# Kernel tuning notes

Hardware: AMD Instinct MI355X
Metric: run time of the kernel (lower is better)

The kernel has to match this reference:

```python
import jax, jax.numpy as jnp
import numpy as np

EPS = 1e-12  # F.normalize eps

def _l2norm(x, axis=-1):
    n = jnp.linalg.norm(x, axis=axis, keepdims=True)
    return x / jnp.maximum(n, EPS)

def setup_inputs() -> dict:
    key = jax.random.key(0)
    k1, k2 = jax.random.split(key)
    Q, D = 512, 1024
    B, L = 64, 1024
    queries = jax.random.normal(k1, (Q, D), dtype=jnp.float32)
    local_tokens = jax.random.normal(k2, (B, L, D), dtype=jnp.float32)
    return {"queries": queries, "local_tokens": local_tokens}

def reference(queries, local_tokens):
    # sim_op == 'dot', repeat == True, need_attn_weights == False
    D = local_tokens.shape[-1]
    denom = jnp.sqrt(jnp.asarray(D, dtype=queries.dtype))
    # scores: [B, Q, L] == bmm(expand(queries), local_tokens^T) / sqrt(D)
    scores = jnp.einsum('qd,bld->bql', queries, local_tokens) / denom
    attn = jax.nn.softmax(scores, axis=-1)
    # aggregated: [B, Q, D]
    agg = jnp.einsum('bql,bld->bqd', attn, local_tokens)
    # post L2-normalize both sides (query normalize is batch-invariant)
    qn = _l2norm(queries)          # [Q, D]
    aggn = _l2norm(agg)            # [B, Q, D]
    # per-(b,q) dot product -> [B, Q], then transpose -> [Q, B]
    logits = jnp.einsum('qd,bqd->bq', qn, aggn).T
    return logits
```

## Files before the change

### kernel.cpp

```cpp
#include <hip/hip_runtime.h>
#include <stdint.h>

#define QN 512
#define DN 1024
#define BN 64
#define LN 1024

typedef _Float16 f16x8 __attribute__((ext_vector_type(8)));
typedef _Float16 f16x4 __attribute__((ext_vector_type(4)));
typedef float f32x4 __attribute__((ext_vector_type(4)));

#define DMA16(gp, lp)                                                        \
  __builtin_amdgcn_global_load_lds(                                          \
      (const __attribute__((address_space(1))) uint32_t*)(const void*)(gp),  \
      (__attribute__((address_space(3))) uint32_t*)(void*)(lp), 16, 0, 0)

#define WAITVM0() asm volatile("s_waitcnt vmcnt(0)" ::: "memory")

__global__ __launch_bounds__(256) void k_convert(const float* __restrict__ tok,
                                                 _Float16* __restrict__ T,
                                                 _Float16* __restrict__ TT) {
  __shared__ __align__(16) _Float16 tile[64][68];
  const int b = blockIdx.z;
  const int l0 = blockIdx.y * 64, d0 = blockIdx.x * 64;
  const int tid = threadIdx.x;
  const int rr = tid >> 4;
  const int cq = tid & 15;
  const size_t base = (size_t)b * LN * DN;
#pragma unroll
  for (int p = 0; p < 4; ++p) {
    const int l = p * 16 + rr;
    const float4 v = *(const float4*)(tok + base + (size_t)(l0 + l) * DN + d0 + cq * 4);
    f16x4 hv;
    hv[0] = (_Float16)v.x; hv[1] = (_Float16)v.y; hv[2] = (_Float16)v.z; hv[3] = (_Float16)v.w;
    *(f16x4*)(T + base + (size_t)(l0 + l) * DN + d0 + cq * 4) = hv;
    tile[cq * 4 + 0][l] = hv[0];
    tile[cq * 4 + 1][l] = hv[1];
    tile[cq * 4 + 2][l] = hv[2];
    tile[cq * 4 + 3][l] = hv[3];
  }
  __syncthreads();
  const size_t baseT = (size_t)b * DN * LN;
#pragma unroll
  for (int p = 0; p < 4; ++p) {
    const int d = p * 16 + rr;
    const f16x4 hv = *(const f16x4*)(&tile[d][cq * 4]);
    *(f16x4*)(TT + baseT + (size_t)(d0 + d) * LN + l0 + cq * 4) = hv;
  }
}

__global__ __launch_bounds__(256) void k_queries(const float* __restrict__ q,
                                                 _Float16* __restrict__ Qh,
                                                 float* __restrict__ invqn) {
  const int qr = blockIdx.x;
  const int tid = threadIdx.x;
  const float4 v = *(const float4*)(q + (size_t)qr * DN + tid * 4);
  float ss = v.x * v.x + v.y * v.y + v.z * v.z + v.w * v.w;
#pragma unroll
  for (int off = 1; off < 64; off <<= 1) ss += __shfl_xor(ss, off, 64);
  __shared__ float red[4];
  if ((tid & 63) == 0) red[tid >> 6] = ss;
  __syncthreads();
  const float tot = red[0] + red[1] + red[2] + red[3];
  f16x4 hv;
  hv[0] = (_Float16)v.x; hv[1] = (_Float16)v.y; hv[2] = (_Float16)v.z; hv[3] = (_Float16)v.w;
  *(f16x4*)(Qh + (size_t)qr * DN + tid * 4) = hv;
  if (tid == 0) invqn[qr] = 1.0f / fmaxf(sqrtf(tot), 1e-12f);
}

__device__ __forceinline__ void decode_bq(int g, int& b, int& q0) {
  const int xcd = g & 7;
  const int t = g >> 3;
  const int qt8 = t & 7;
  b = ((t >> 3) << 3) | xcd;
  q0 = qt8 * 64;
}

__global__ __launch_bounds__(512, 2) void k_scores(const _Float16* __restrict__ Qh,
                                                   const _Float16* __restrict__ T,
                                                   _Float16* __restrict__ P,
                                                   float* __restrict__ numv) {
  __shared__ __align__(16) _Float16 Bb[2][32768];
  __shared__ __align__(16) _Float16 As[2][2048];
  __shared__ float maxbuf[8][64];
  __shared__ float sumbuf[8][64];
  __shared__ float numbuf[8][64];
  __shared__ float Mbuf[64];
  __shared__ float Rbuf[64];
  int b, q0;
  decode_bq(blockIdx.x, b, q0);
  const int tid = threadIdx.x;
  const int w = tid >> 6, lane = tid & 63, c = lane & 15, quad = lane >> 4;

  const char* __restrict__ gT = (const char*)(T + (size_t)b * LN * DN);
  const char* __restrict__ gA = (const char*)(Qh + (size_t)q0 * DN);

  const int r4 = lane >> 2;
  const int qsw = ((lane & 3) - ((lane >> 3) & 3)) & 3;
  const char* gBbase = gT + (size_t)(w * 128 + r4) * 2048 + qsw * 16;
  const char* gAbase = gA + (size_t)(w * 16 + r4) * 2048 + qsw * 16;

  const int bswz = ((quad + ((c >> 1) & 3)) & 3) * 8;
  const int boff = (w * 128 + c) * 32 + bswz;
  const int aoff = c * 32 + bswz;

  f32x4 acc[4][8];
#pragma unroll
  for (int i = 0; i < 4; ++i)
#pragma unroll
    for (int j = 0; j < 8; ++j) acc[i][j] = 0.f;

#pragma unroll
  for (int j = 0; j < 8; ++j) DMA16(gBbase + j * 32768, &Bb[0][(w * 8 + j) * 512]);
  if (w < 4) DMA16(gAbase, &As[0][w * 512]);
  WAITVM0();
  __syncthreads();

  for (int s = 0; s < 32; ++s) {
    const int cur = s & 1;
    if (s < 31) {
      const int sn = s + 1;
#pragma unroll
      for (int j = 0; j < 8; ++j)
        DMA16(gBbase + j * 32768 + sn * 64, &Bb[cur ^ 1][(w * 8 + j) * 512]);
      if (w < 4) DMA16(gAbase + sn * 64, &As[cur ^ 1][w * 512]);
    }

    const _Float16* __restrict__ Bp = &Bb[cur][0];
    const _Float16* __restrict__ Ap = &As[cur][0];
    f16x8 afr[4];
#pragma unroll
    for (int qt = 0; qt < 4; ++qt) afr[qt] = *(const f16x8*)(Ap + aoff + qt * 512);
#pragma unroll
    for (int lt = 0; lt < 8; ++lt) {
      const f16x8 bv = *(const f16x8*)(Bp + boff + lt * 512);
#pragma unroll
      for (int qt = 0; qt < 4; ++qt)
        acc[qt][lt] = __builtin_amdgcn_mfma_f32_16x16x32_f16(afr[qt], bv, acc[qt][lt], 0, 0, 0);
    }
    WAITVM0();
    __syncthreads();
  }

  float mx[4][4];
#pragma unroll
  for (int qt = 0; qt < 4; ++qt)
#pragma unroll
    for (int r = 0; r < 4; ++r) {
      float m = acc[qt][0][r];
#pragma unroll
      for (int lt = 1; lt < 8; ++lt) m = fmaxf(m, acc[qt][lt][r]);
      mx[qt][r] = m;
    }
#pragma unroll
  for (int off = 1; off < 16; off <<= 1)
#pragma unroll
    for (int qt = 0; qt < 4; ++qt)
#pragma unroll
      for (int r = 0; r < 4; ++r) mx[qt][r] = fmaxf(mx[qt][r], __shfl_xor(mx[qt][r], off, 64));
  if (c == 0)
#pragma unroll
    for (int qt = 0; qt < 4; ++qt)
#pragma unroll
      for (int r = 0; r < 4; ++r) maxbuf[w][qt * 16 + quad * 4 + r] = mx[qt][r];
  __syncthreads();
  if (tid < 64) {
    float m = maxbuf[0][tid];
#pragma unroll
    for (int ww = 1; ww < 8; ++ww) m = fmaxf(m, maxbuf[ww][tid]);
    Mbuf[tid] = m;
  }
  __syncthreads();

  const float KE = 0.045084220027780106f;
  float Mr[4][4], sl[4][4], nl[4][4];
#pragma unroll
  for (int qt = 0; qt < 4; ++qt)
#pragma unroll
    for (int r = 0; r < 4; ++r) {
      Mr[qt][r] = Mbuf[qt * 16 + quad * 4 + r];
      sl[qt][r] = 0.f;
      nl[qt][r] = 0.f;
    }
#pragma unroll
  for (int qt = 0; qt < 4; ++qt)
#pragma unroll
    for (int lt = 0; lt < 8; ++lt)
#pragma unroll
      for (int r = 0; r < 4; ++r) {
        const float u = acc[qt][lt][r];
        const float p = exp2f((u - Mr[qt][r]) * KE);
        acc[qt][lt][r] = p;
        sl[qt][r] += p;
        nl[qt][r] += p * u;
      }
#pragma unroll
  for (int off = 1; off < 16; off <<= 1)
#pragma unroll
    for (int qt = 0; qt < 4; ++qt)
#pragma unroll
      for (int r = 0; r < 4; ++r) {
        sl[qt][r] += __shfl_xor(sl[qt][r], off, 64);
        nl[qt][r] += __shfl_xor(nl[qt][r], off, 64);
      }
  if (c == 0)
#pragma unroll
    for (int qt = 0; qt < 4; ++qt)
#pragma unroll
      for (int r = 0; r < 4; ++r) {
        sumbuf[w][qt * 16 + quad * 4 + r] = sl[qt][r];
        numbuf[w][qt * 16 + quad * 4 + r] = nl[qt][r];
      }
  __syncthreads();
  if (tid < 64) {
    float S = 0.f, N = 0.f;
#pragma unroll
    for (int ww = 0; ww < 8; ++ww) {
      S += sumbuf[ww][tid];
      N += numbuf[ww][tid];
    }
    Rbuf[tid] = 1.0f / S;
    numv[(size_t)b * QN + q0 + tid] = N / S;
  }
  __syncthreads();

  _Float16* Pb = P + ((size_t)b * QN + q0) * LN;
#pragma unroll
  for (int qt = 0; qt < 4; ++qt)
#pragma unroll
    for (int r = 0; r < 4; ++r) {
      const int row = qt * 16 + quad * 4 + r;
      const float rS = Rbuf[row];
      _Float16* prow = Pb + (size_t)row * LN + c;
#pragma unroll
      for (int lt = 0; lt < 8; ++lt) prow[w * 128 + lt * 16] = (_Float16)(acc[qt][lt][r] * rS);
    }
}

__global__ __launch_bounds__(512, 2) void k_agg(const _Float16* __restrict__ P,
                                                const _Float16* __restrict__ TT,
                                                float* __restrict__ norm2) {
  __shared__ __align__(16) _Float16 Bb[2][32768];
  __shared__ __align__(16) _Float16 As[2][2048];
  __shared__ float redbuf[8][64];
  int b, q0;
  decode_bq(blockIdx.x, b, q0);
  const int tid = threadIdx.x;
  const int w = tid >> 6, lane = tid & 63, c = lane & 15, quad = lane >> 4;

  const char* __restrict__ gT = (const char*)(TT + (size_t)b * DN * LN);
  const char* __restrict__ gA = (const char*)(P + ((size_t)b * QN + q0) * LN);

  const int r4 = lane >> 2;
  const int qsw = ((lane & 3) - ((lane >> 3) & 3)) & 3;
  const char* gBbase = gT + (size_t)(w * 128 + r4) * 2048 + qsw * 16;
  const char* gAbase = gA + (size_t)(w * 16 + r4) * 2048 + qsw * 16;

  const int bswz = ((quad + ((c >> 1) & 3)) & 3) * 8;
  const int boff = (w * 128 + c) * 32 + bswz;
  const int aoff = c * 32 + bswz;

  f32x4 acc[4][8];
#pragma unroll
  for (int i = 0; i < 4; ++i)
#pragma unroll
    for (int j = 0; j < 8; ++j) acc[i][j] = 0.f;

#pragma unroll
  for (int j = 0; j < 8; ++j) DMA16(gBbase + j * 32768, &Bb[0][(w * 8 + j) * 512]);
  if (w < 4) DMA16(gAbase, &As[0][w * 512]);
  WAITVM0();
  __syncthreads();

  for (int s = 0; s < 32; ++s) {
    const int cur = s & 1;
    if (s < 31) {
      const int sn = s + 1;
#pragma unroll
      for (int j = 0; j < 8; ++j)
        DMA16(gBbase + j * 32768 + sn * 64, &Bb[cur ^ 1][(w * 8 + j) * 512]);
      if (w < 4) DMA16(gAbase + sn * 64, &As[cur ^ 1][w * 512]);
    }

    const _Float16* __restrict__ Bp = &Bb[cur][0];
    const _Float16* __restrict__ Ap = &As[cur][0];
    f16x8 afr[4];
#pragma unroll
    for (int qt = 0; qt < 4; ++qt) afr[qt] = *(const f16x8*)(Ap + aoff + qt * 512);
#pragma unroll
    for (int dt = 0; dt < 8; ++dt) {
      const f16x8 bv = *(const f16x8*)(Bp + boff + dt * 512);
#pragma unroll
      for (int qt = 0; qt < 4; ++qt)
        acc[qt][dt] = __builtin_amdgcn_mfma_f32_16x16x32_f16(afr[qt], bv, acc[qt][dt], 0, 0, 0);
    }
    WAITVM0();
    __syncthreads();
  }

  float ss[4][4];
#pragma unroll
  for (int qt = 0; qt < 4; ++qt)
#pragma unroll
    for (int r = 0; r < 4; ++r) {
      float s = 0.f;
#pragma unroll
      for (int dt = 0; dt < 8; ++dt) {
        const float v = acc[qt][dt][r];
        s += v * v;
      }
      ss[qt][r] = s;
    }
#pragma unroll
  for (int off = 1; off < 16; off <<= 1)
#pragma unroll
    for (int qt = 0; qt < 4; ++qt)
#pragma unroll
      for (int r = 0; r < 4; ++r) ss[qt][r] += __shfl_xor(ss[qt][r], off, 64);
  if (c == 0)
#pragma unroll
    for (int qt = 0; qt < 4; ++qt)
#pragma unroll
      for (int r = 0; r < 4; ++r) redbuf[w][qt * 16 + quad * 4 + r] = ss[qt][r];
  __syncthreads();
  if (tid < 64) {
    float s = 0.f;
#pragma unroll
    for (int ww = 0; ww < 8; ++ww) s += redbuf[ww][tid];
    norm2[(size_t)b * QN + q0 + tid] = s;
  }
}

__global__ __launch_bounds__(256) void k_final(const float* __restrict__ numv,
                                               const float* __restrict__ norm2,
                                               const float* __restrict__ invqn,
                                               float* __restrict__ out) {
  const int idx = blockIdx.x * 256 + threadIdx.x;
  const int q = idx >> 6, b = idx & 63;
  const float n = numv[(size_t)b * QN + q];
  const float d = sqrtf(norm2[(size_t)b * QN + q]);
  out[idx] = n * invqn[q] / fmaxf(d, 1e-12f);
}

extern "C" void kernel_launch(void* const* d_in, const int* in_sizes, int n_in,
                              void* d_out, int out_size, void* d_ws, size_t ws_size,
                              hipStream_t stream) {
  (void)in_sizes; (void)n_in; (void)out_size; (void)ws_size;
  const float* queries = (const float*)d_in[0];
  const float* tok = (const float*)d_in[1];
  float* out = (float*)d_out;
  char* ws = (char*)d_ws;

  _Float16* TT = (_Float16*)(ws + 0);
  _Float16* T = (_Float16*)(ws + 134217728);
  _Float16* P = (_Float16*)(ws + 268435456);
  _Float16* Qh = (_Float16*)(ws + 335544320);
  float* invqn = (float*)(ws + 336592896);
  float* numv = (float*)(ws + 336594944);
  float* norm2 = (float*)(ws + 336726016);

  hipLaunchKernelGGL(k_convert, dim3(16, 16, 64), dim3(256), 0, stream, tok, T, TT);
  hipLaunchKernelGGL(k_queries, dim3(512), dim3(256), 0, stream, queries, Qh, invqn);
  hipLaunchKernelGGL(k_scores, dim3(512), dim3(512), 0, stream, Qh, T, P, numv);
  hipLaunchKernelGGL(k_agg, dim3(512), dim3(512), 0, stream, P, TT, norm2);
  hipLaunchKernelGGL(k_final, dim3(128), dim3(256), 0, stream, numv, norm2, invqn, out);
}
```

Before: 701.7 us.

## Load A fragments into registers and drop block barriers in GEMM loops

In both k_scores and k_agg, the shared-memory staging of the A operand is replaced by direct per-lane global loads into registers, prefetched one step ahead. Each wave already loads and reads only its own slice of the B tile, so the per-iteration __syncthreads and the full vmcnt(0) wait give way to per-wave waits (lgkmcnt(0) before overwriting LDS, vmcnt(12) before consuming). The last K step is peeled out of the loop. This is meant to remove block-wide barrier stalls and let waves drift relative to each other, at the cost of more global load instructions per lane and reliance on exact waitcnt counting for correctness.

```diff
diff --git a/kernel.cpp b/kernel.cpp
--- a/kernel.cpp
+++ b/kernel.cpp
@@ -14,8 +14,6 @@
   __builtin_amdgcn_global_load_lds(                                          \
       (const __attribute__((address_space(1))) uint32_t*)(const void*)(gp),  \
       (__attribute__((address_space(3))) uint32_t*)(void*)(lp), 16, 0, 0)
-
-#define WAITVM0() asm volatile("s_waitcnt vmcnt(0)" ::: "memory")
 
 __global__ __launch_bounds__(256) void k_convert(const float* __restrict__ tok,
                                                  _Float16* __restrict__ T,
@@ -81,7 +79,6 @@
                                                    _Float16* __restrict__ P,
                                                    float* __restrict__ numv) {
   __shared__ __align__(16) _Float16 Bb[2][32768];
-  __shared__ __align__(16) _Float16 As[2][2048];
   __shared__ float maxbuf[8][64];
   __shared__ float sumbuf[8][64];
   __shared__ float numbuf[8][64];
@@ -93,16 +90,14 @@
   const int w = tid >> 6, lane = tid & 63, c = lane & 15, quad = lane >> 4;
 
   const char* __restrict__ gT = (const char*)(T + (size_t)b * LN * DN);
-  const char* __restrict__ gA = (const char*)(Qh + (size_t)q0 * DN);
+  const _Float16* __restrict__ gA = Qh + (size_t)q0 * DN;
 
   const int r4 = lane >> 2;
   const int qsw = ((lane & 3) - ((lane >> 3) & 3)) & 3;
   const char* gBbase = gT + (size_t)(w * 128 + r4) * 2048 + qsw * 16;
-  const char* gAbase = gA + (size_t)(w * 16 + r4) * 2048 + qsw * 16;
 
   const int bswz = ((quad + ((c >> 1) & 3)) & 3) * 8;
   const int boff = (w * 128 + c) * 32 + bswz;
-  const int aoff = c * 32 + bswz;
 
   f32x4 acc[4][8];
 #pragma unroll
@@ -110,36 +105,49 @@
 #pragma unroll
     for (int j = 0; j < 8; ++j) acc[i][j] = 0.f;
 
-#pragma unroll
-  for (int j = 0; j < 8; ++j) DMA16(gBbase + j * 32768, &Bb[0][(w * 8 + j) * 512]);
-  if (w < 4) DMA16(gAbase, &As[0][w * 512]);
-  WAITVM0();
-  __syncthreads();
-
-  for (int s = 0; s < 32; ++s) {
+  const _Float16* gAl = gA + (size_t)c * DN + quad * 8;
+
+  f16x8 a_cur[4], a_nxt[4];
+#pragma unroll
+  for (int qt = 0; qt < 4; ++qt) a_cur[qt] = *(const f16x8*)(gAl + (size_t)qt * 16 * DN);
+#pragma unroll
+  for (int j = 0; j < 8; ++j) DMA16(gBbase + (size_t)j * 32768, &Bb[0][(w * 8 + j) * 512]);
+
+  for (int s = 0; s < 31; ++s) {
     const int cur = s & 1;
-    if (s < 31) {
-      const int sn = s + 1;
-#pragma unroll
-      for (int j = 0; j < 8; ++j)
-        DMA16(gBbase + j * 32768 + sn * 64, &Bb[cur ^ 1][(w * 8 + j) * 512]);
-      if (w < 4) DMA16(gAbase + sn * 64, &As[cur ^ 1][w * 512]);
-    }
+    const int sn = s + 1;
+#pragma unroll
+    for (int qt = 0; qt < 4; ++qt)
+      a_nxt[qt] = *(const f16x8*)(gAl + (size_t)qt * 16 * DN + sn * 32);
+    asm volatile("s_waitcnt lgkmcnt(0)" ::: "memory");
+#pragma unroll
+    for (int j = 0; j < 8; ++j)
+      DMA16(gBbase + (size_t)j * 32768 + sn * 64, &Bb[cur ^ 1][(w * 8 + j) * 512]);
+    asm volatile("s_waitcnt vmcnt(12)" ::: "memory");
+    __builtin_amdgcn_sched_barrier(0);
 
     const _Float16* __restrict__ Bp = &Bb[cur][0];
-    const _Float16* __restrict__ Ap = &As[cur][0];
-    f16x8 afr[4];
-#pragma unroll
-    for (int qt = 0; qt < 4; ++qt) afr[qt] = *(const f16x8*)(Ap + aoff + qt * 512);
 #pragma unroll
     for (int lt = 0; lt < 8; ++lt) {
       const f16x8 bv = *(const f16x8*)(Bp + boff + lt * 512);
 #pragma unroll
       for (int qt = 0; qt < 4; ++qt)
-        acc[qt][lt] = __builtin_amdgcn_mfma_f32_16x16x32_f16(afr[qt], bv, acc[qt][lt], 0, 0, 0);
-    }
-    WAITVM0();
-    __syncthreads();
+        acc[qt][lt] = __builtin_amdgcn_mfma_f32_16x16x32_f16(a_cur[qt], bv, acc[qt][lt], 0, 0, 0);
+    }
+#pragma unroll
+    for (int qt = 0; qt < 4; ++qt) a_cur[qt] = a_nxt[qt];
+  }
+  asm volatile("s_waitcnt vmcnt(0)" ::: "memory");
+  __builtin_amdgcn_sched_barrier(0);
+  {
+    const _Float16* __restrict__ Bp = &Bb[1][0];
+#pragma unroll
+    for (int lt = 0; lt < 8; ++lt) {
+      const f16x8 bv = *(const f16x8*)(Bp + boff + lt * 512);
+#pragma unroll
+      for (int qt = 0; qt < 4; ++qt)
+        acc[qt][lt] = __builtin_amdgcn_mfma_f32_16x16x32_f16(a_cur[qt], bv, acc[qt][lt], 0, 0, 0);
+    }
   }
 
   float mx[4][4];
@@ -241,7 +249,6 @@
                                                 const _Float16* __restrict__ TT,
                                                 float* __restrict__ norm2) {
   __shared__ __align__(16) _Float16 Bb[2][32768];
-  __shared__ __align__(16) _Float16 As[2][2048];
   __shared__ float redbuf[8][64];
   int b, q0;
   decode_bq(blockIdx.x, b, q0);
@@ -249,16 +256,14 @@
   const int w = tid >> 6, lane = tid & 63, c = lane & 15, quad = lane >> 4;
 
   const char* __restrict__ gT = (const char*)(TT + (size_t)b * DN * LN);
-  const char* __restrict__ gA = (const char*)(P + ((size_t)b * QN + q0) * LN);
+  const _Float16* __restrict__ gA = P + ((size_t)b * QN + q0) * LN;
 
   const int r4 = lane >> 2;
   const int qsw = ((lane & 3) - ((lane >> 3) & 3)) & 3;
   const char* gBbase = gT + (size_t)(w * 128 + r4) * 2048 + qsw * 16;
-  const char* gAbase = gA + (size_t)(w * 16 + r4) * 2048 + qsw * 16;
 
   const int bswz = ((quad + ((c >> 1) & 3)) & 3) * 8;
   const int boff = (w * 128 + c) * 32 + bswz;
-  const int aoff = c * 32 + bswz;
 
   f32x4 acc[4][8];
 #pragma unroll
@@ -266,36 +271,49 @@
 #pragma unroll
     for (int j = 0; j < 8; ++j) acc[i][j] = 0.f;
 
-#pragma unroll
-  for (int j = 0; j < 8; ++j) DMA16(gBbase + j * 32768, &Bb[0][(w * 8 + j) * 512]);
-  if (w < 4) DMA16(gAbase, &As[0][w * 512]);
-  WAITVM0();
-  __syncthreads();
-
-  for (int s = 0; s < 32; ++s) {
+  const _Float16* gAl = gA + (size_t)c * LN + quad * 8;
+
+  f16x8 a_cur[4], a_nxt[4];
+#pragma unroll
+  for (int qt = 0; qt < 4; ++qt) a_cur[qt] = *(const f16x8*)(gAl + (size_t)qt * 16 * LN);
+#pragma unroll
+  for (int j = 0; j < 8; ++j) DMA16(gBbase + (size_t)j * 32768, &Bb[0][(w * 8 + j) * 512]);
+
+  for (int s = 0; s < 31; ++s) {
     const int cur = s & 1;
-    if (s < 31) {
-      const int sn = s + 1;
-#pragma unroll
-      for (int j = 0; j < 8; ++j)
-        DMA16(gBbase + j * 32768 + sn * 64, &Bb[cur ^ 1][(w * 8 + j) * 512]);
-      if (w < 4) DMA16(gAbase + sn * 64, &As[cur ^ 1][w * 512]);
-    }
+    const int sn = s + 1;
+#pragma unroll
+    for (int qt = 0; qt < 4; ++qt)
+      a_nxt[qt] = *(const f16x8*)(gAl + (size_t)qt * 16 * LN + sn * 32);
+    asm volatile("s_waitcnt lgkmcnt(0)" ::: "memory");
+#pragma unroll
+    for (int j = 0; j < 8; ++j)
+      DMA16(gBbase + (size_t)j * 32768 + sn * 64, &Bb[cur ^ 1][(w * 8 + j) * 512]);
+    asm volatile("s_waitcnt vmcnt(12)" ::: "memory");
+    __builtin_amdgcn_sched_barrier(0);
 
     const _Float16* __restrict__ Bp = &Bb[cur][0];
-    const _Float16* __restrict__ Ap = &As[cur][0];
-    f16x8 afr[4];
-#pragma unroll
-    for (int qt = 0; qt < 4; ++qt) afr[qt] = *(const f16x8*)(Ap + aoff + qt * 512);
 #pragma unroll
     for (int dt = 0; dt < 8; ++dt) {
       const f16x8 bv = *(const f16x8*)(Bp + boff + dt * 512);
 #pragma unroll
       for (int qt = 0; qt < 4; ++qt)
-        acc[qt][dt] = __builtin_amdgcn_mfma_f32_16x16x32_f16(afr[qt], bv, acc[qt][dt], 0, 0, 0);
-    }
-    WAITVM0();
-    __syncthreads();
+        acc[qt][dt] = __builtin_amdgcn_mfma_f32_16x16x32_f16(a_cur[qt], bv, acc[qt][dt], 0, 0, 0);
+    }
+#pragma unroll
+    for (int qt = 0; qt < 4; ++qt) a_cur[qt] = a_nxt[qt];
+  }
+  asm volatile("s_waitcnt vmcnt(0)" ::: "memory");
+  __builtin_amdgcn_sched_barrier(0);
+  {
+    const _Float16* __restrict__ Bp = &Bb[1][0];
+#pragma unroll
+    for (int dt = 0; dt < 8; ++dt) {
+      const f16x8 bv = *(const f16x8*)(Bp + boff + dt * 512);
+#pragma unroll
+      for (int qt = 0; qt < 4; ++qt)
+        acc[qt][dt] = __builtin_amdgcn_mfma_f32_16x16x32_f16(a_cur[qt], bv, acc[qt][dt], 0, 0, 0);
+    }
   }
 
   float ss[4][4];
```

New measurement: 680.7 us. 1.03x faster.
